# Performance work log

Measured on AMD Instinct MI355X. Metric: run time of the kernel, lower is better.

Reference implementation:

```python
import jax, jax.numpy as jnp
import numpy as np

T, D, H, E, K = 8192, 1024, 4096, 8, 2


def setup_inputs() -> dict:
    key = jax.random.key(0)
    ks = jax.random.split(key, 6)
    s_in = 1.0 / np.sqrt(D)
    s_hid = 1.0 / np.sqrt(H)
    return {
        "hidden_states": jax.random.normal(ks[0], (T, D), dtype=jnp.float32),
        "router_w": jax.random.normal(ks[1], (D, E), dtype=jnp.float32) * s_in,
        "expert_w1": jax.random.normal(ks[2], (E, D, H), dtype=jnp.float32) * s_in,
        "expert_w2": jax.random.normal(ks[3], (E, H, D), dtype=jnp.float32) * s_hid,
        "shared_w1": jax.random.normal(ks[4], (D, H), dtype=jnp.float32) * s_in,
        "shared_w2": jax.random.normal(ks[5], (H, D), dtype=jnp.float32) * s_hid,
    }


def reference(hidden_states, router_w, expert_w1, expert_w2, shared_w1, shared_w2):
    x = hidden_states  # [T, D]
    # --- router: softmax over experts, keep top-k, renormalize ---
    probs = jax.nn.softmax(x @ router_w, axis=-1)            # [T, E]
    top_v, top_i = jax.lax.top_k(probs, K)                   # [T, K]
    top_v = top_v / jnp.sum(top_v, axis=-1, keepdims=True)
    # dense combine weights [T, E]; zero for non-selected experts
    comb = jnp.zeros((x.shape[0], E), x.dtype).at[
        jnp.arange(x.shape[0])[:, None], top_i].set(top_v)
    # --- routed experts (dense reference for grouped GEMM) ---
    h = jax.nn.silu(jnp.einsum('td,edh->eth', x, expert_w1))  # [E, T, H]
    eo = jnp.einsum('eth,ehd->etd', h, expert_w2)             # [E, T, D]
    routed = jnp.einsum('te,etd->td', comb, eo)               # [T, D]
    # --- shared expert, always active ---
    shared = jax.nn.silu(x @ shared_w1) @ shared_w2           # [T, D]
    return routed + shared
```

## Files before the change

kernel.cpp:

```cpp
#include <hip/hip_runtime.h>
#include <hip/hip_bf16.h>
#include <stdint.h>

typedef unsigned short u16;
typedef __attribute__((ext_vector_type(8))) short bf16x8;
typedef __attribute__((ext_vector_type(4))) float f32x4;

constexpr int T_ = 8192;
constexpr int D_ = 1024;
constexpr int H_ = 4096;
constexpr int E_ = 8;
constexpr int MAXROWS = 25600;
constexpr int NTILES  = 200;

__device__ __forceinline__ unsigned int f2bf_bits(float f) {
  unsigned int u = __float_as_uint(f);
  return (u + 0x7fffu + ((u >> 16) & 1u)) >> 16;
}

__device__ __forceinline__ void load_lds16(const void* g, void* s) {
  __builtin_amdgcn_global_load_lds(
      (const __attribute__((address_space(1))) unsigned int*)g,
      (__attribute__((address_space(3))) unsigned int*)s, 16, 0, 0);
}

__global__ __launch_bounds__(256) void router_kernel(
    const float* __restrict__ x, const float* __restrict__ rw,
    int* __restrict__ counts, int* __restrict__ tok2, float* __restrict__ wgt2) {
  __shared__ float rw_s[E_ * D_];
  __shared__ int c_s[E_];
  const int tid = threadIdx.x;
  if (tid < E_) c_s[tid] = 0;
  for (int f = tid; f < 2048; f += 256) {
    int d = f >> 1, p = f & 1;
    float4 v = *(const float4*)(rw + d * 8 + p * 4);
    rw_s[(p * 4 + 0) * D_ + d] = v.x;
    rw_s[(p * 4 + 1) * D_ + d] = v.y;
    rw_s[(p * 4 + 2) * D_ + d] = v.z;
    rw_s[(p * 4 + 3) * D_ + d] = v.w;
  }
  __syncthreads();
  const int wid = tid >> 6, lane = tid & 63;
  for (int ti = 0; ti < 16; ++ti) {
    const int t = blockIdx.x * 64 + wid * 16 + ti;
    const float* xr = x + (long)t * D_;
    float acc[E_] = {0.f, 0.f, 0.f, 0.f, 0.f, 0.f, 0.f, 0.f};
    for (int j = 0; j < 16; ++j) {
      const int d = lane + 64 * j;
      const float xv = xr[d];
#pragma unroll
      for (int e = 0; e < E_; ++e) acc[e] += xv * rw_s[e * D_ + d];
    }
#pragma unroll
    for (int off = 32; off >= 1; off >>= 1) {
#pragma unroll
      for (int e = 0; e < E_; ++e) acc[e] += __shfl_xor(acc[e], off, 64);
    }
    if (lane == 0) {
      int i0 = 0; float l0 = acc[0];
#pragma unroll
      for (int e = 1; e < E_; ++e) if (acc[e] > l0) { l0 = acc[e]; i0 = e; }
      int i1 = -1; float l1 = -3.4e38f;
#pragma unroll
      for (int e = 0; e < E_; ++e) if (e != i0 && acc[e] > l1) { l1 = acc[e]; i1 = e; }
      const float r = __expf(l1 - l0);
      const float inv = 1.f / (1.f + r);
      tok2[2 * t] = i0; tok2[2 * t + 1] = i1;
      wgt2[2 * t] = inv; wgt2[2 * t + 1] = r * inv;
      atomicAdd(&c_s[i0], 1); atomicAdd(&c_s[i1], 1);
    }
  }
  __syncthreads();
  if (tid < E_) atomicAdd(&counts[tid], c_s[tid]);
}

__global__ void scan_kernel(const int* __restrict__ counts, int* __restrict__ offs,
                            int* __restrict__ tile_expert, int* __restrict__ rowtok) {
  __shared__ int so[10];
  const int tid = threadIdx.x;
  if (tid == 0) {
    int o = 0;
    for (int e = 0; e < E_; ++e) { so[e] = o; o += ((counts[e] + 127) >> 7) << 7; }
    so[8] = o;
    o += T_;
    so[9] = o;
    for (int i = 0; i < 10; ++i) offs[i] = so[i];
  }
  __syncthreads();
  for (int i = tid; i < NTILES; i += 256) {
    const int row = i << 7;
    int e = 8;
    if (row < so[8]) {
      e = 7;
      for (int k = 0; k < 7; ++k) if (row < so[k + 1]) { e = k; break; }
    }
    tile_expert[i] = e;
  }
  for (int r = tid; r < MAXROWS; r += 256) rowtok[r] = 0;
}

__global__ __launch_bounds__(256) void assign_kernel(
    const int* __restrict__ tok2, const int* __restrict__ offs,
    int* __restrict__ cursors, int* __restrict__ rowtok, int* __restrict__ pos2) {
  __shared__ int lcnt[E_], lbase[E_];
  const int tid = threadIdx.x;
  if (tid < E_) lcnt[tid] = 0;
  __syncthreads();
  const int t = blockIdx.x * 256 + tid;
  const int e0 = tok2[2 * t], e1 = tok2[2 * t + 1];
  const int s0 = atomicAdd(&lcnt[e0], 1);
  const int s1 = atomicAdd(&lcnt[e1], 1);
  __syncthreads();
  if (tid < E_) lbase[tid] = offs[tid] + atomicAdd(&cursors[tid], lcnt[tid]);
  __syncthreads();
  const int p0 = lbase[e0] + s0, p1 = lbase[e1] + s1;
  rowtok[p0] = t; rowtok[p1] = t;
  pos2[2 * t] = p0; pos2[2 * t + 1] = p1;
  rowtok[offs[8] + t] = t;
}

__global__ __launch_bounds__(256) void cvt_x_kernel(const float* __restrict__ x,
                                                    u16* __restrict__ xb) {
  const long i = ((long)blockIdx.x * 256 + threadIdx.x) * 4;
  const float4 v = *(const float4*)(x + i);
  ushort4 o;
  o.x = (u16)f2bf_bits(v.x); o.y = (u16)f2bf_bits(v.y);
  o.z = (u16)f2bf_bits(v.z); o.w = (u16)f2bf_bits(v.w);
  *(ushort4*)(xb + i) = o;
}

__global__ __launch_bounds__(256) void transpose_cvt_kernel(
    const float* __restrict__ src8, const float* __restrict__ srcShared,
    u16* __restrict__ dst, int R, int C) {
  __shared__ float tile[64][65];
  const long stride = (long)R * C;
  const float* src = (blockIdx.z < 8) ? src8 + (long)blockIdx.z * stride : srcShared;
  u16* d = dst + (long)blockIdx.z * stride;
  const int tid = threadIdx.x;
  const int r0 = blockIdx.y * 64, c0 = blockIdx.x * 64;
  const int lr = tid >> 4, lc4 = tid & 15;
#pragma unroll
  for (int p = 0; p < 4; ++p) {
    const float4 v = *(const float4*)(src + (long)(r0 + lr + 16 * p) * C + c0 + lc4 * 4);
    tile[lr + 16 * p][lc4 * 4 + 0] = v.x;
    tile[lr + 16 * p][lc4 * 4 + 1] = v.y;
    tile[lr + 16 * p][lc4 * 4 + 2] = v.z;
    tile[lr + 16 * p][lc4 * 4 + 3] = v.w;
  }
  __syncthreads();
#pragma unroll
  for (int p = 0; p < 4; ++p) {
    const int rr = lr + 16 * p;
    ushort4 o;
    o.x = (u16)f2bf_bits(tile[lc4 * 4 + 0][rr]);
    o.y = (u16)f2bf_bits(tile[lc4 * 4 + 1][rr]);
    o.z = (u16)f2bf_bits(tile[lc4 * 4 + 2][rr]);
    o.w = (u16)f2bf_bits(tile[lc4 * 4 + 3][rr]);
    *(ushort4*)(d + (long)(c0 + rr) * R + r0 + lc4 * 4) = o;
  }
}

template <bool G1, int CHM>
__global__ __launch_bounds__(256) void moe_gemm(
    const u16* __restrict__ A, const u16* __restrict__ Bt, void* __restrict__ C,
    const int* __restrict__ rowtok, const int* __restrict__ tile_expert) {
  constexpr int K = G1 ? 1024 : 4096;
  constexpr int N = G1 ? 4096 : 1024;
  constexpr int NT = N / 128;
  constexpr int NIT = K / 32;
  __shared__ u16 As[3 * 4096];
  __shared__ u16 Bs[3 * 4096];

  const int tid = threadIdx.x;
  int mt, nt;
  {
    const int bid = blockIdx.x;
    const int cb = CHM * NT;
    const int chunk = bid / cb;
    const int mt0 = chunk * CHM;
    const int m = min(CHM, NTILES - mt0);
    const int rem = bid - chunk * cb;
    mt = mt0 + rem % m;
    nt = rem / m;
  }
  const int e = tile_expert[mt];

  const int sr = tid >> 2;
  const int sc = (((tid & 3) ^ ((sr >> 1) & 3)) << 3);

  long aoff0, aoff1;
  if constexpr (G1) {
    aoff0 = (long)rowtok[mt * 128 + sr] * K;
    aoff1 = (long)rowtok[mt * 128 + 64 + sr] * K;
  } else {
    aoff0 = (long)(mt * 128 + sr) * K;
    aoff1 = (long)(mt * 128 + 64 + sr) * K;
  }
  const u16* pa0 = A + aoff0 + sc;
  const u16* pa1 = A + aoff1 + sc;
  const u16* pb0 = Bt + (long)e * N * K + (long)(nt * 128 + sr) * K + sc;
  const u16* pb1 = pb0 + (long)64 * K;

  const int lane = tid & 63;
  const int wid = tid >> 6;
  const int wm = (wid >> 1) * 64;
  const int wn = (wid & 1) * 64;
  const int lr = lane & 15;
  const int quad = lane >> 4;
  const int cA = ((quad ^ ((lr >> 1) & 3)) << 3);

  f32x4 acc[4][4] = {};

  auto stage = [&](int b, int koff) {
    u16* a_d = As + b * 4096 + tid * 8;
    u16* b_d = Bs + b * 4096 + tid * 8;
    load_lds16(pa0 + koff, a_d);
    load_lds16(pa1 + koff, a_d + 2048);
    load_lds16(pb0 + koff, b_d);
    load_lds16(pb1 + koff, b_d + 2048);
  };
  auto compute = [&](int b) {
    const u16* a_s = As + b * 4096;
    const u16* b_s = Bs + b * 4096;
    bf16x8 af[4], bfv[4];
#pragma unroll
    for (int i = 0; i < 4; ++i)
      af[i] = *(const bf16x8*)(a_s + (wm + i * 16 + lr) * 32 + cA);
#pragma unroll
    for (int j2 = 0; j2 < 4; ++j2)
      bfv[j2] = *(const bf16x8*)(b_s + (wn + j2 * 16 + lr) * 32 + cA);
    __builtin_amdgcn_s_setprio(1);
#pragma unroll
    for (int i = 0; i < 4; ++i)
#pragma unroll
      for (int j2 = 0; j2 < 4; ++j2)
        acc[i][j2] =
            __builtin_amdgcn_mfma_f32_16x16x32_bf16(af[i], bfv[j2], acc[i][j2], 0, 0, 0);
    __builtin_amdgcn_s_setprio(0);
  };

  stage(0, 0);
  asm volatile("" ::: "memory");
  stage(1, 32);

  int cur = 0;
#pragma unroll 1
  for (int j = 0; j < NIT - 1; ++j) {
    asm volatile("s_waitcnt vmcnt(4)\n\ts_barrier" ::: "memory");
    if (j + 2 < NIT) {
      const int nb = (cur == 0) ? 2 : cur - 1;
      stage(nb, (j + 2) * 32);
    }
    compute(cur);
    cur = (cur == 2) ? 0 : cur + 1;
  }
  asm volatile("s_waitcnt vmcnt(0)\n\ts_barrier" ::: "memory");
  compute(cur);

  const int rbase = mt * 128 + wm + quad * 4;
  if constexpr (G1) {
    u16* Hout = (u16*)C;
#pragma unroll
    for (int i = 0; i < 4; ++i) {
#pragma unroll
      for (int j = 0; j < 4; ++j) {
#pragma unroll
        for (int r = 0; r < 4; ++r) {
          float v = acc[i][j][r];
          v = v / (1.f + __expf(-v));
          unsigned int u = f2bf_bits(v);
          unsigned int other = (unsigned int)__shfl_xor((int)u, 1, 64);
          if (!(lane & 1)) {
            const unsigned int w = (u & 0xffffu) | (other << 16);
            const long row = rbase + i * 16 + r;
            const int col = nt * 128 + wn + j * 16 + lr;
            *(unsigned int*)(Hout + row * N + col) = w;
          }
        }
      }
    }
  } else {
    float* O = (float*)C;
#pragma unroll
    for (int i = 0; i < 4; ++i)
#pragma unroll
      for (int j = 0; j < 4; ++j)
#pragma unroll
        for (int r = 0; r < 4; ++r) {
          const long row = rbase + i * 16 + r;
          const int col = nt * 128 + wn + j * 16 + lr;
          O[row * N + col] = acc[i][j][r];
        }
  }
}

__global__ __launch_bounds__(256) void combine_kernel(
    const float* __restrict__ eo, const int* __restrict__ pos2,
    const float* __restrict__ wgt2, const int* __restrict__ offs,
    float* __restrict__ out) {
  const int t = blockIdx.x, tid = threadIdx.x;
  const int p0 = pos2[2 * t], p1 = pos2[2 * t + 1];
  const float w0 = wgt2[2 * t], w1 = wgt2[2 * t + 1];
  const int ps = offs[8] + t;
  const long c = (long)tid * 4;
  const float4 a = *(const float4*)(eo + (long)p0 * D_ + c);
  const float4 b = *(const float4*)(eo + (long)p1 * D_ + c);
  const float4 s = *(const float4*)(eo + (long)ps * D_ + c);
  float4 o;
  o.x = w0 * a.x + w1 * b.x + s.x;
  o.y = w0 * a.y + w1 * b.y + s.y;
  o.z = w0 * a.z + w1 * b.z + s.z;
  o.w = w0 * a.w + w1 * b.w + s.w;
  *(float4*)(out + (long)t * D_ + c) = o;
}

extern "C" void kernel_launch(void* const* d_in, const int* in_sizes, int n_in,
                              void* d_out, int out_size, void* d_ws, size_t ws_size,
                              hipStream_t stream) {
  const float* x   = (const float*)d_in[0];
  const float* rw  = (const float*)d_in[1];
  const float* w1  = (const float*)d_in[2];
  const float* w2  = (const float*)d_in[3];
  const float* sw1 = (const float*)d_in[4];
  const float* sw2 = (const float*)d_in[5];
  float* out = (float*)d_out;

  char* ws = (char*)d_ws;
  int*   counts      = (int*)(ws + 0);
  int*   cursors     = (int*)(ws + 64);
  int*   offs        = (int*)(ws + 128);
  int*   tile_expert = (int*)(ws + 192);
  int*   tok2        = (int*)(ws + 4096);
  float* wgt2        = (float*)(ws + 4096 + 65536);
  int*   pos2        = (int*)(ws + 4096 + 131072);
  int*   rowtok      = (int*)(ws + 4096 + 196608);

  size_t off = 1u << 20;
  u16* xb  = (u16*)(ws + off); off += (size_t)T_ * D_ * 2;
  u16* w1t = (u16*)(ws + off); off += (size_t)9 * H_ * D_ * 2;
  u16* w2t = (u16*)(ws + off); off += (size_t)9 * D_ * H_ * 2;
  u16* h   = (u16*)(ws + off); off += (size_t)MAXROWS * H_ * 2;
  float* eo = (float*)(ws + off); off += (size_t)MAXROWS * D_ * 4;

  hipMemsetAsync(ws, 0, 256, stream);
  router_kernel<<<128, 256, 0, stream>>>(x, rw, counts, tok2, wgt2);
  scan_kernel<<<1, 256, 0, stream>>>(counts, offs, tile_expert, rowtok);
  assign_kernel<<<32, 256, 0, stream>>>(tok2, offs, cursors, rowtok, pos2);
  cvt_x_kernel<<<T_ * D_ / 1024, 256, 0, stream>>>(x, xb);
  transpose_cvt_kernel<<<dim3(H_ / 64, D_ / 64, 9), 256, 0, stream>>>(w1, sw1, w1t, D_, H_);
  transpose_cvt_kernel<<<dim3(D_ / 64, H_ / 64, 9), 256, 0, stream>>>(w2, sw2, w2t, H_, D_);
  moe_gemm<true, 24><<<NTILES * (H_ / 128), 256, 0, stream>>>(xb, w1t, h, rowtok, tile_expert);
  moe_gemm<false, 64><<<NTILES * (D_ / 128), 256, 0, stream>>>(h, w2t, eo, rowtok, tile_expert);
  combine_kernel<<<T_, 256, 0, stream>>>(eo, pos2, wgt2, offs, out);
}
```

Measured before the change: 1.043 ms.

## Widen MoE GEMM tile to 128x256 with split-phase B staging

```diff
diff --git a/kernel.cpp b/kernel.cpp
--- a/kernel.cpp
+++ b/kernel.cpp
@@ -161,15 +161,15 @@
 }
 
 template <bool G1, int CHM>
-__global__ __launch_bounds__(256) void moe_gemm(
+__global__ __launch_bounds__(256, 2) void moe_gemm(
     const u16* __restrict__ A, const u16* __restrict__ Bt, void* __restrict__ C,
     const int* __restrict__ rowtok, const int* __restrict__ tile_expert) {
   constexpr int K = G1 ? 1024 : 4096;
   constexpr int N = G1 ? 4096 : 1024;
-  constexpr int NT = N / 128;
+  constexpr int NT = N / 256;
   constexpr int NIT = K / 32;
   __shared__ u16 As[3 * 4096];
-  __shared__ u16 Bs[3 * 4096];
+  __shared__ u16 Bs[3 * 8192];
 
   const int tid = threadIdx.x;
   int mt, nt;
@@ -198,64 +198,83 @@
   }
   const u16* pa0 = A + aoff0 + sc;
   const u16* pa1 = A + aoff1 + sc;
-  const u16* pb0 = Bt + (long)e * N * K + (long)(nt * 128 + sr) * K + sc;
-  const u16* pb1 = pb0 + (long)64 * K;
+  const u16* pb = Bt + (long)e * N * K + (long)(nt * 256 + sr) * K + sc;
 
   const int lane = tid & 63;
   const int wid = tid >> 6;
   const int wm = (wid >> 1) * 64;
-  const int wn = (wid & 1) * 64;
+  const int wn = (wid & 1) * 128;
   const int lr = lane & 15;
   const int quad = lane >> 4;
   const int cA = ((quad ^ ((lr >> 1) & 3)) << 3);
 
-  f32x4 acc[4][4] = {};
-
-  auto stage = [&](int b, int koff) {
+  f32x4 acc[4][8] = {};
+
+  auto stageA = [&](int b, int koff) {
     u16* a_d = As + b * 4096 + tid * 8;
-    u16* b_d = Bs + b * 4096 + tid * 8;
     load_lds16(pa0 + koff, a_d);
     load_lds16(pa1 + koff, a_d + 2048);
-    load_lds16(pb0 + koff, b_d);
-    load_lds16(pb1 + koff, b_d + 2048);
+    load_lds16(pb + koff, Bs + b * 8192 + tid * 8);
   };
-  auto compute = [&](int b) {
-    const u16* a_s = As + b * 4096;
-    const u16* b_s = Bs + b * 4096;
-    bf16x8 af[4], bfv[4];
+  auto stageB = [&](int b, int koff) {
+    u16* b_d = Bs + b * 8192 + tid * 8;
+    load_lds16(pb + (long)64 * K + koff, b_d + 2048);
+    load_lds16(pb + (long)128 * K + koff, b_d + 4096);
+    load_lds16(pb + (long)192 * K + koff, b_d + 6144);
+  };
+
+  stageA(0, 0); stageB(0, 0);
+  asm volatile("" ::: "memory");
+  stageA(1, 32); stageB(1, 32);
+  asm volatile("s_waitcnt vmcnt(6)\n\ts_barrier" ::: "memory");
+
+  int cur = 0;
+#pragma unroll 1
+  for (int t = 0; t < NIT; ++t) {
+    const int kst = (t + 2) * 32;
+    const bool st = (t + 2 < NIT);
+    const int nb = (cur == 0) ? 2 : cur - 1;
+    const u16* a_s = As + cur * 4096;
+    const u16* b_s = Bs + cur * 8192;
+    bf16x8 af[4], bv[4];
+
 #pragma unroll
     for (int i = 0; i < 4; ++i)
       af[i] = *(const bf16x8*)(a_s + (wm + i * 16 + lr) * 32 + cA);
 #pragma unroll
-    for (int j2 = 0; j2 < 4; ++j2)
-      bfv[j2] = *(const bf16x8*)(b_s + (wn + j2 * 16 + lr) * 32 + cA);
+    for (int j = 0; j < 4; ++j)
+      bv[j] = *(const bf16x8*)(b_s + (wn + j * 16 + lr) * 32 + cA);
+    if (st) stageA(nb, kst);
+    asm volatile("s_barrier" ::: "memory");
+    asm volatile("s_waitcnt lgkmcnt(0)" ::: "memory");
     __builtin_amdgcn_s_setprio(1);
 #pragma unroll
     for (int i = 0; i < 4; ++i)
 #pragma unroll
-      for (int j2 = 0; j2 < 4; ++j2)
-        acc[i][j2] =
-            __builtin_amdgcn_mfma_f32_16x16x32_bf16(af[i], bfv[j2], acc[i][j2], 0, 0, 0);
+      for (int j = 0; j < 4; ++j)
+        acc[i][j] = __builtin_amdgcn_mfma_f32_16x16x32_bf16(af[i], bv[j], acc[i][j], 0, 0, 0);
     __builtin_amdgcn_s_setprio(0);
-  };
-
-  stage(0, 0);
-  asm volatile("" ::: "memory");
-  stage(1, 32);
-
-  int cur = 0;
-#pragma unroll 1
-  for (int j = 0; j < NIT - 1; ++j) {
-    asm volatile("s_waitcnt vmcnt(4)\n\ts_barrier" ::: "memory");
-    if (j + 2 < NIT) {
-      const int nb = (cur == 0) ? 2 : cur - 1;
-      stage(nb, (j + 2) * 32);
-    }
-    compute(cur);
+    asm volatile("s_barrier" ::: "memory");
+
+#pragma unroll
+    for (int j = 0; j < 4; ++j)
+      bv[j] = *(const bf16x8*)(b_s + (wn + (j + 4) * 16 + lr) * 32 + cA);
+    if (st) stageB(nb, kst);
+    asm volatile("s_barrier" ::: "memory");
+    asm volatile("s_waitcnt lgkmcnt(0)" ::: "memory");
+    __builtin_amdgcn_s_setprio(1);
+#pragma unroll
+    for (int i = 0; i < 4; ++i)
+#pragma unroll
+      for (int j = 0; j < 4; ++j)
+        acc[i][j + 4] = __builtin_amdgcn_mfma_f32_16x16x32_bf16(af[i], bv[j], acc[i][j + 4], 0, 0, 0);
+    __builtin_amdgcn_s_setprio(0);
+    if (t < NIT - 1) {
+      if (st) asm volatile("s_waitcnt vmcnt(6)\n\ts_barrier" ::: "memory");
+      else    asm volatile("s_waitcnt vmcnt(0)\n\ts_barrier" ::: "memory");
+    }
     cur = (cur == 2) ? 0 : cur + 1;
   }
-  asm volatile("s_waitcnt vmcnt(0)\n\ts_barrier" ::: "memory");
-  compute(cur);
 
   const int rbase = mt * 128 + wm + quad * 4;
   if constexpr (G1) {
@@ -263,7 +282,7 @@
 #pragma unroll
     for (int i = 0; i < 4; ++i) {
 #pragma unroll
-      for (int j = 0; j < 4; ++j) {
+      for (int j = 0; j < 8; ++j) {
 #pragma unroll
         for (int r = 0; r < 4; ++r) {
           float v = acc[i][j][r];
@@ -273,7 +292,7 @@
           if (!(lane & 1)) {
             const unsigned int w = (u & 0xffffu) | (other << 16);
             const long row = rbase + i * 16 + r;
-            const int col = nt * 128 + wn + j * 16 + lr;
+            const int col = nt * 256 + wn + j * 16 + lr;
             *(unsigned int*)(Hout + row * N + col) = w;
           }
         }
@@ -284,11 +303,11 @@
 #pragma unroll
     for (int i = 0; i < 4; ++i)
 #pragma unroll
-      for (int j = 0; j < 4; ++j)
+      for (int j = 0; j < 8; ++j)
 #pragma unroll
         for (int r = 0; r < 4; ++r) {
           const long row = rbase + i * 16 + r;
-          const int col = nt * 128 + wn + j * 16 + lr;
+          const int col = nt * 256 + wn + j * 16 + lr;
           O[row * N + col] = acc[i][j][r];
         }
   }
@@ -349,7 +368,7 @@
   cvt_x_kernel<<<T_ * D_ / 1024, 256, 0, stream>>>(x, xb);
   transpose_cvt_kernel<<<dim3(H_ / 64, D_ / 64, 9), 256, 0, stream>>>(w1, sw1, w1t, D_, H_);
   transpose_cvt_kernel<<<dim3(D_ / 64, H_ / 64, 9), 256, 0, stream>>>(w2, sw2, w2t, H_, D_);
-  moe_gemm<true, 24><<<NTILES * (H_ / 128), 256, 0, stream>>>(xb, w1t, h, rowtok, tile_expert);
-  moe_gemm<false, 64><<<NTILES * (D_ / 128), 256, 0, stream>>>(h, w2t, eo, rowtok, tile_expert);
+  moe_gemm<true, 32><<<NTILES * (H_ / 256), 256, 0, stream>>>(xb, w1t, h, rowtok, tile_expert);
+  moe_gemm<false, 128><<<NTILES * (D_ / 256), 256, 0, stream>>>(h, w2t, eo, rowtok, tile_expert);
   combine_kernel<<<T_, 256, 0, stream>>>(eo, pos2, wgt2, offs, out);
 }
```

Result: no change. 1.024 ms (-1.8%).
